# Kernel tuning notes

Hardware: AMD Instinct MI355X
Metric: run time of the kernel (lower is better)

## Reference

```python
import jax, jax.numpy as jnp
import numpy as np

B, N, D, F = 4, 4096, 1024, 64
LN_EPS = 1e-5
ATTN_EPS = 1e-6


def setup_inputs() -> dict:
    key = jax.random.key(0)
    ks = jax.random.split(key, 9)
    s = 0.02  # small init scale for weights
    return {
        "x": jax.random.normal(ks[0], (B, N, D), dtype=jnp.float32),
        "ln1_w": jnp.ones((D,), jnp.float32),
        "ln1_b": jnp.zeros((D,), jnp.float32),
        "q_w": jax.random.normal(ks[1], (F, D), jnp.float32) * s,
        "q_b": jnp.zeros((F,), jnp.float32),
        "k_w": jax.random.normal(ks[2], (F, D), jnp.float32) * s,
        "k_b": jnp.zeros((F,), jnp.float32),
        "v_w": jax.random.normal(ks[3], (D, D), jnp.float32) * s,
        "v_b": jnp.zeros((D,), jnp.float32),
        "o_w": jax.random.normal(ks[4], (D, D), jnp.float32) * s,
        "o_b": jnp.zeros((D,), jnp.float32),
        "ln2_w": jnp.ones((D,), jnp.float32),
        "ln2_b": jnp.zeros((D,), jnp.float32),
        "f1_w": jax.random.normal(ks[5], (4 * D, D), jnp.float32) * s,
        "f1_b": jnp.zeros((4 * D,), jnp.float32),
        "f2_w": jax.random.normal(ks[6], (D, 4 * D), jnp.float32) * s,
        "f2_b": jnp.zeros((D,), jnp.float32),
    }


def _layer_norm(x, w, b):
    mu = jnp.mean(x, axis=-1, keepdims=True)
    var = jnp.var(x, axis=-1, keepdims=True)
    return (x - mu) * jax.lax.rsqrt(var + LN_EPS) * w + b


def _linear(x, w, b):
    # torch nn.Linear convention: y = x @ w.T + b, w: [out, in]
    return jnp.einsum('bnd,fd->bnf', x, w) + b


def _causal_linear_attn(Q, K, V, eps=ATTN_EPS):
    """Q,K: [B,N,F] positive features; V: [B,N,D]. Recurrent causal scan."""
    b, n, f = K.shape
    d = V.shape[-1]
    Qt = jnp.swapaxes(Q, 0, 1)  # [N,B,F]
    Kt = jnp.swapaxes(K, 0, 1)
    Vt = jnp.swapaxes(V, 0, 1)  # [N,B,D]

    def step(carry, qkv):
        KV, Ks = carry  # [B,F,D], [B,F]
        q, k, v = qkv
        KV = KV + k[:, :, None] * v[:, None, :]
        Ks = Ks + k
        num = jnp.einsum('bf,bfd->bd', q, KV)
        den = jnp.sum(q * Ks, axis=-1, keepdims=True) + eps
        return (KV, Ks), num / den

    init = (jnp.zeros((b, f, d), Q.dtype), jnp.zeros((b, f), Q.dtype))
    _, out = jax.lax.scan(step, init, (Qt, Kt, Vt))
    return jnp.swapaxes(out, 0, 1)  # [B,N,D]


def reference(x, ln1_w, ln1_b, q_w, q_b, k_w, k_b, v_w, v_b,
              o_w, o_b, ln2_w, ln2_b, f1_w, f1_b, f2_w, f2_b):
    x_norm = _layer_norm(x, ln1_w, ln1_b)
    # LinearHopfieldASA, causal=True
    Q = jax.nn.elu(_linear(x_norm, q_w, q_b)) + 1.0  # positive feature map
    K = jax.nn.elu(_linear(x_norm, k_w, k_b)) + 1.0
    V = _linear(x_norm, v_w, v_b)
    attn = _causal_linear_attn(Q, K, V)
    attn = _linear(attn, o_w, o_b)
    x = x + attn
    h = _layer_norm(x, ln2_w, ln2_b)
    h = jax.nn.gelu(_linear(h, f1_w, f1_b), approximate=False)
    x = x + _linear(h, f2_w, f2_b)
    return x
```

## Files before the change

### kernel.cpp

```cpp
#include <hip/hip_runtime.h>
#include <hip/hip_bf16.h>
#include <cstdint>
#include <cstddef>


typedef __attribute__((ext_vector_type(8))) short short8;
typedef __attribute__((ext_vector_type(4))) short short4v;
typedef __attribute__((ext_vector_type(4))) float floatx4;
typedef __attribute__((ext_vector_type(4))) unsigned short ushort4v;

#define DEV static __device__ __forceinline__

DEV float b2f(unsigned short u) {
    union { unsigned int i; float f; } v; v.i = ((unsigned int)u) << 16; return v.f;
}
DEV unsigned short f2b(float f) {
    union { float f; unsigned int i; } v; v.f = f;
    unsigned int i = v.i;
    unsigned int r = (i + 0x7FFFu + ((i >> 16) & 1u)) >> 16;
    return (unsigned short)r;
}

DEV void gl_lds16(const void* g, void* l) {
    __builtin_amdgcn_global_load_lds((const __attribute__((address_space(1))) void*)g,
                                     (__attribute__((address_space(3))) void*)l, 16, 0, 0);
}

__global__ void eel_prep(const float* __restrict__ qw, const float* __restrict__ kw,
                         const float* __restrict__ vw, const float* __restrict__ ow,
                         const float* __restrict__ f1w, const float* __restrict__ f2w,
                         const float* __restrict__ qb, const float* __restrict__ kb,
                         const float* __restrict__ vb,
                         uint16_t* __restrict__ Wqkv, uint16_t* __restrict__ Wo,
                         uint16_t* __restrict__ W1, uint16_t* __restrict__ W2,
                         float* __restrict__ bqkv)
{
    size_t i = (size_t)blockIdx.x * 256 + threadIdx.x;
    size_t stride = (size_t)gridDim.x * 256;
    for (size_t t = i; t < 1152u * 1024u; t += stride) {
        int r = (int)(t >> 10);
        float v = (r < 64) ? qw[t] : (r < 128) ? kw[t - 65536] : vw[t - 131072];
        Wqkv[t] = f2b(v);
    }
    for (size_t t = i; t < 1048576u; t += stride) Wo[t] = f2b(ow[t]);
    for (size_t t = i; t < 4194304u; t += stride) { W1[t] = f2b(f1w[t]); W2[t] = f2b(f2w[t]); }
    if (i < 1152) bqkv[i] = (i < 64) ? qb[i] : (i < 128) ? kb[i - 64] : vb[i - 128];
}

__global__ __launch_bounds__(256) void eel_ln(const float* __restrict__ x,
                                              const float* __restrict__ w,
                                              const float* __restrict__ b,
                                              uint16_t* __restrict__ out)
{
    int row = blockIdx.x, tid = threadIdx.x;
    float4 xv = ((const float4*)(x + (size_t)row * 1024))[tid];
    float s  = xv.x + xv.y + xv.z + xv.w;
    float s2 = xv.x*xv.x + xv.y*xv.y + xv.z*xv.z + xv.w*xv.w;
#pragma unroll
    for (int off = 32; off > 0; off >>= 1) {
        s  += __shfl_down(s, off);
        s2 += __shfl_down(s2, off);
    }
    __shared__ float ps[8];
    int wv = tid >> 6;
    if ((tid & 63) == 0) { ps[wv] = s; ps[4 + wv] = s2; }
    __syncthreads();
    float mu  = (ps[0] + ps[1] + ps[2] + ps[3]) * (1.0f / 1024.0f);
    float var = (ps[4] + ps[5] + ps[6] + ps[7]) * (1.0f / 1024.0f) - mu * mu;
    float rs = rsqrtf(var + 1e-5f);
    float4 wv4 = ((const float4*)w)[tid];
    float4 bv4 = ((const float4*)b)[tid];
    ushort4v o;
    o.x = f2b((xv.x - mu) * rs * wv4.x + bv4.x);
    o.y = f2b((xv.y - mu) * rs * wv4.y + bv4.y);
    o.z = f2b((xv.z - mu) * rs * wv4.z + bv4.z);
    o.w = f2b((xv.w - mu) * rs * wv4.w + bv4.w);
    *(ushort4v*)(out + (size_t)row * 1024 + tid * 4) = o;
}

#define BM 128
#define BN 128
#define BKK 64

__global__ __launch_bounds__(256, 2) void eel_gemm(
    const uint16_t* __restrict__ A, int lda,
    const uint16_t* __restrict__ Bm, int ldb,
    int K,
    const float* __restrict__ bias,
    const float* __restrict__ res,
    uint16_t* __restrict__ outb,
    float* __restrict__ outf,
    int ldc, int mode)
{
    __shared__ uint16_t As[BM * BKK];
    __shared__ uint16_t Bs[BN * BKK];
    int tid = threadIdx.x;
    int lane = tid & 63, w = tid >> 6;
    int m0 = blockIdx.x * BM, n0 = blockIdx.y * BN;
    int wr = (w >> 1) * 64, wc = (w & 1) * 64;
    int quad = lane >> 4, l16 = lane & 15;
    floatx4 acc[4][4] = {};

    int nkb = K / BKK;
    for (int kb = 0; kb < nkb; ++kb) {
        int k0 = kb * BKK;
#pragma unroll
        for (int it = 0; it < 4; ++it) {
            int seg = it * 256 + tid;
            int row = seg >> 3, sub = seg & 7;
            int gs = sub ^ (row & 7);
            gl_lds16(A + (size_t)(m0 + row) * lda + k0 + gs * 8, (char*)As + seg * 16);
            gl_lds16(Bm + (size_t)(n0 + row) * ldb + k0 + gs * 8, (char*)Bs + seg * 16);
        }
        __syncthreads();
#pragma unroll
        for (int ks = 0; ks < 2; ++ks) {
            short8 a[4], b[4];
#pragma unroll
            for (int i = 0; i < 4; i++) {
                int mrow = wr + i * 16 + l16;
                int sa = (ks * 4 + quad) ^ (mrow & 7);
                a[i] = *(const short8*)((const char*)As + mrow * (BKK * 2) + sa * 16);
                int nrow = wc + i * 16 + l16;
                int sb = (ks * 4 + quad) ^ (nrow & 7);
                b[i] = *(const short8*)((const char*)Bs + nrow * (BKK * 2) + sb * 16);
            }
#pragma unroll
            for (int i = 0; i < 4; i++)
#pragma unroll
                for (int j = 0; j < 4; j++)
                    acc[i][j] = __builtin_amdgcn_mfma_f32_16x16x32_bf16(a[i], b[j], acc[i][j], 0, 0, 0);
        }
        __syncthreads();
    }

#pragma unroll
    for (int j = 0; j < 4; j++) {
        int col = n0 + wc + j * 16 + l16;
        float bv = bias[col];
#pragma unroll
        for (int i = 0; i < 4; i++) {
#pragma unroll
            for (int r = 0; r < 4; r++) {
                int row = m0 + wr + i * 16 + quad * 4 + r;
                float v = acc[i][j][r] + bv;
                size_t off = (size_t)row * ldc + col;
                if (mode == 0) {
                    if (col < 128) v = (v > 0.f) ? v + 1.f : __expf(v);
                    outb[off] = f2b(v);
                } else if (mode == 1) {
                    outf[off] = v + res[off];
                } else {
                    float u = 0.7978845608028654f * v * (1.0f + 0.044715f * v * v);
                    float e = __expf(2.0f * u);
                    float t = 1.0f - 2.0f / (e + 1.0f);
                    v = 0.5f * v * (1.0f + t);
                    outb[off] = f2b(v);
                }
            }
        }
    }
}

__global__ __launch_bounds__(256) void eel_attn_s(
    const uint16_t* __restrict__ QKV,
    uint16_t* __restrict__ Sg,
    float* __restrict__ den,
    float* __restrict__ KsA)
{
    int chunk = blockIdx.x, tid = threadIdx.x;
    int tok0 = chunk * 64;
    __shared__ uint16_t Q[64 * 64];
    __shared__ uint16_t Kc[64 * 64];
    __shared__ float denp[64][4];
    {
        int nloc = tid >> 2, seg = tid & 3;
        const uint16_t* src = QKV + (size_t)(tok0 + nloc) * 1152 + seg * 16;
        *(short8*)(Q + nloc * 64 + seg * 16)     = *(const short8*)(src);
        *(short8*)(Q + nloc * 64 + seg * 16 + 8) = *(const short8*)(src + 8);
        src += 64;
        *(short8*)(Kc + nloc * 64 + seg * 16)     = *(const short8*)(src);
        *(short8*)(Kc + nloc * 64 + seg * 16 + 8) = *(const short8*)(src + 8);
    }
    __syncthreads();
    if (tid < 64) {
        float s = 0.f;
        for (int m = 0; m < 64; m++) s += b2f(Kc[m * 64 + tid]);
        KsA[chunk * 64 + tid] = s;
    }
    int n = tid >> 2, mg = tid & 3;
    float dsum = 0.f;
    for (int mi = 0; mi < 16; mi++) {
        int m = mg * 16 + mi;
        size_t soff = (size_t)(tok0 + n) * 64 + m;
        if (m <= n) {
            float s = 0.f;
#pragma unroll
            for (int f = 0; f < 64; f += 8) {
                short8 q8 = *(const short8*)(Q + n * 64 + f);
                short8 k8 = *(const short8*)(Kc + m * 64 + f);
#pragma unroll
                for (int j = 0; j < 8; j++)
                    s += b2f((unsigned short)q8[j]) * b2f((unsigned short)k8[j]);
            }
            dsum += s;
            Sg[soff] = f2b(s);
        } else {
            Sg[soff] = 0;
        }
    }
    denp[n][mg] = dsum;
    __syncthreads();
    if (tid < 64)
        den[tok0 + tid] = denp[tid][0] + denp[tid][1] + denp[tid][2] + denp[tid][3];
}

__global__ __launch_bounds__(256) void eel_attn_kv(
    const uint16_t* __restrict__ QKV,
    float* __restrict__ KV_A)
{
    int bi = blockIdx.x;
    int chunk = bi >> 3, p = bi & 7;
    int tid = threadIdx.x;
    int tok0 = chunk * 64;
    __shared__ uint16_t Kc[64 * 64];
    __shared__ uint16_t Vp[64 * 128];
    {
        int r = tid >> 2, sg = tid & 3;
        const uint16_t* src = QKV + (size_t)(tok0 + r) * 1152 + 64 + sg * 16;
        *(short8*)(Kc + r * 64 + sg * 16)     = *(const short8*)(src);
        *(short8*)(Kc + r * 64 + sg * 16 + 8) = *(const short8*)(src + 8);
    }
#pragma unroll
    for (int it = 0; it < 2; it++) {
        int s = it * 256 + tid;
        int r = s >> 3, sub = s & 7;
        const uint16_t* src = QKV + (size_t)(tok0 + r) * 1152 + 128 + p * 128 + sub * 16;
        *(short8*)(Vp + r * 128 + sub * 16)     = *(const short8*)(src);
        *(short8*)(Vp + r * 128 + sub * 16 + 8) = *(const short8*)(src + 8);
    }
    __syncthreads();
    int f0 = (tid >> 5) * 8, d0 = (tid & 31) * 4;
    float acc[8][4] = {};
#pragma unroll 2
    for (int m = 0; m < 64; m++) {
        short8 k8 = *(const short8*)(Kc + m * 64 + f0);
        short4v v4 = *(const short4v*)(Vp + m * 128 + d0);
        float v0 = b2f((unsigned short)v4[0]), v1 = b2f((unsigned short)v4[1]);
        float v2 = b2f((unsigned short)v4[2]), v3 = b2f((unsigned short)v4[3]);
#pragma unroll
        for (int i = 0; i < 8; i++) {
            float kk = b2f((unsigned short)k8[i]);
            acc[i][0] += kk * v0; acc[i][1] += kk * v1;
            acc[i][2] += kk * v2; acc[i][3] += kk * v3;
        }
    }
#pragma unroll
    for (int i = 0; i < 8; i++) {
        float4 st = { acc[i][0], acc[i][1], acc[i][2], acc[i][3] };
        *(float4*)(KV_A + ((size_t)chunk * 64 + f0 + i) * 1024 + p * 128 + d0) = st;
    }
}

__global__ __launch_bounds__(256) void eel_kv_prefix(
    const float* __restrict__ KV_A, uint16_t* __restrict__ KV_P)
{
    int bi = blockIdx.x;
    int b = bi >> 8, rem = bi & 255;
    int f = rem >> 2;
    int d = (rem & 3) * 256 + threadIdx.x;
    float acc = 0.f;
    for (int cc = 0; cc < 64; cc++) {
        size_t idx = (((size_t)(b * 64 + cc)) * 64 + f) * 1024 + d;
        KV_P[idx] = f2b(acc);
        acc += KV_A[idx];
    }
}

__global__ void eel_ks_prefix(const float* __restrict__ KsA, float* __restrict__ KsP)
{
    int b = blockIdx.x, f = threadIdx.x;
    float acc = 0.f;
    for (int cc = 0; cc < 64; cc++) {
        int idx = (b * 64 + cc) * 64 + f;
        KsP[idx] = acc;
        acc += KsA[idx];
    }
}

__global__ __launch_bounds__(256) void eel_attn_out(
    const uint16_t* __restrict__ QKV,
    const uint16_t* __restrict__ Sg,
    const float* __restrict__ den,
    const float* __restrict__ KsP,
    const uint16_t* __restrict__ KV_P,
    uint16_t* __restrict__ attn)
{
    int bi = blockIdx.x;
    int chunk = bi >> 3, p = bi & 7;
    int tid = threadIdx.x;
    int tok0 = chunk * 64;
    __shared__ uint16_t Qt[64 * 64];
    __shared__ uint16_t St[64 * 64];
    __shared__ uint16_t Vp[64 * 128];
    __shared__ uint16_t KVp[64 * 128];
    __shared__ float dfull[64];
    {
        int n = tid >> 2, fs = (tid & 3) * 16;
        const uint16_t* qsrc = QKV + (size_t)(tok0 + n) * 1152 + fs;
        short8 a0 = *(const short8*)(qsrc);
        short8 a1 = *(const short8*)(qsrc + 8);
        const uint16_t* ssrc = Sg + (size_t)(tok0 + n) * 64 + fs;
        short8 s0 = *(const short8*)(ssrc);
        short8 s1 = *(const short8*)(ssrc + 8);
#pragma unroll
        for (int j = 0; j < 8; j++) {
            Qt[(fs + j) * 64 + n]     = (unsigned short)a0[j];
            Qt[(fs + 8 + j) * 64 + n] = (unsigned short)a1[j];
            St[(fs + j) * 64 + n]     = (unsigned short)s0[j];
            St[(fs + 8 + j) * 64 + n] = (unsigned short)s1[j];
        }
    }
#pragma unroll
    for (int it = 0; it < 2; it++) {
        int s = it * 256 + tid;
        int r = s >> 3, sub = s & 7;
        const uint16_t* vsrc = QKV + (size_t)(tok0 + r) * 1152 + 128 + p * 128 + sub * 16;
        *(short8*)(Vp + r * 128 + sub * 16)     = *(const short8*)(vsrc);
        *(short8*)(Vp + r * 128 + sub * 16 + 8) = *(const short8*)(vsrc + 8);
        const uint16_t* kvsrc = KV_P + ((size_t)(chunk * 64 + r)) * 1024 + p * 128 + sub * 16;
        *(short8*)(KVp + r * 128 + sub * 16)     = *(const short8*)(kvsrc);
        *(short8*)(KVp + r * 128 + sub * 16 + 8) = *(const short8*)(kvsrc + 8);
    }
    __syncthreads();
    if (tid < 64) {
        float s = 0.f;
        for (int f = 0; f < 64; f++)
            s += b2f(Qt[f * 64 + tid]) * KsP[chunk * 64 + f];
        dfull[tid] = s + den[tok0 + tid] + 1e-6f;
    }
    __syncthreads();
    int n0 = (tid >> 5) * 8, d0 = (tid & 31) * 4;
    float acc[8][4] = {};
#pragma unroll 2
    for (int f = 0; f < 64; f++) {
        short8 q8 = *(const short8*)(Qt + f * 64 + n0);
        short4v kv4 = *(const short4v*)(KVp + f * 128 + d0);
        float v0 = b2f((unsigned short)kv4[0]), v1 = b2f((unsigned short)kv4[1]);
        float v2 = b2f((unsigned short)kv4[2]), v3 = b2f((unsigned short)kv4[3]);
#pragma unroll
        for (int i = 0; i < 8; i++) {
            float q = b2f((unsigned short)q8[i]);
            acc[i][0] += q * v0; acc[i][1] += q * v1;
            acc[i][2] += q * v2; acc[i][3] += q * v3;
        }
    }
#pragma unroll 2
    for (int m = 0; m < 64; m++) {
        short8 s8 = *(const short8*)(St + m * 64 + n0);
        short4v v4 = *(const short4v*)(Vp + m * 128 + d0);
        float v0 = b2f((unsigned short)v4[0]), v1 = b2f((unsigned short)v4[1]);
        float v2 = b2f((unsigned short)v4[2]), v3 = b2f((unsigned short)v4[3]);
#pragma unroll
        for (int i = 0; i < 8; i++) {
            float q = b2f((unsigned short)s8[i]);
            acc[i][0] += q * v0; acc[i][1] += q * v1;
            acc[i][2] += q * v2; acc[i][3] += q * v3;
        }
    }
#pragma unroll
    for (int i = 0; i < 8; i++) {
        int n = n0 + i;
        float rinv = 1.0f / dfull[n];
        ushort4v st;
        st.x = f2b(acc[i][0] * rinv);
        st.y = f2b(acc[i][1] * rinv);
        st.z = f2b(acc[i][2] * rinv);
        st.w = f2b(acc[i][3] * rinv);
        *(ushort4v*)(attn + (size_t)(tok0 + n) * 1024 + p * 128 + d0) = st;
    }
}

extern "C" void kernel_launch(void* const* d_in, const int* in_sizes, int n_in,
                              void* d_out, int out_size, void* d_ws, size_t ws_size,
                              hipStream_t stream)
{
    (void)in_sizes; (void)n_in; (void)out_size; (void)ws_size;
    const float* x     = (const float*)d_in[0];
    const float* ln1w  = (const float*)d_in[1];
    const float* ln1b  = (const float*)d_in[2];
    const float* qw    = (const float*)d_in[3];
    const float* qb    = (const float*)d_in[4];
    const float* kw    = (const float*)d_in[5];
    const float* kb    = (const float*)d_in[6];
    const float* vw    = (const float*)d_in[7];
    const float* vb    = (const float*)d_in[8];
    const float* ow    = (const float*)d_in[9];
    const float* ob    = (const float*)d_in[10];
    const float* ln2w  = (const float*)d_in[11];
    const float* ln2b  = (const float*)d_in[12];
    const float* f1w   = (const float*)d_in[13];
    const float* f1b   = (const float*)d_in[14];
    const float* f2w   = (const float*)d_in[15];
    const float* f2bs  = (const float*)d_in[16];
    float* out = (float*)d_out;
    char* ws = (char*)d_ws;

    const size_t o_Wqkv = 0;
    const size_t o_Wo   = o_Wqkv + 2359296;
    const size_t o_W1   = o_Wo   + 2097152;
    const size_t o_W2   = o_W1   + 8388608;
    const size_t o_bqkv = o_W2   + 8388608;
    const size_t O_XN   = 21238272;
    const size_t O_QKV  = 54792704;
    const size_t O_S    = 92541440;
    const size_t O_DEN  = 94638592;
    const size_t O_KSA  = 94704128;
    const size_t O_KSP  = 94769664;
    const size_t O_KVA  = 94835200;
    const size_t O_KVP  = 161944064;

    uint16_t* Wqkv  = (uint16_t*)(ws + o_Wqkv);
    uint16_t* Wo    = (uint16_t*)(ws + o_Wo);
    uint16_t* W1    = (uint16_t*)(ws + o_W1);
    uint16_t* W2    = (uint16_t*)(ws + o_W2);
    float*    bqkv  = (float*)(ws + o_bqkv);
    uint16_t* xn    = (uint16_t*)(ws + O_XN);
    uint16_t* attn  = (uint16_t*)(ws + O_XN);
    uint16_t* QKV   = (uint16_t*)(ws + O_QKV);
    uint16_t* hnorm = (uint16_t*)(ws + O_QKV);
    uint16_t* Sg    = (uint16_t*)(ws + O_S);
    float*    den   = (float*)(ws + O_DEN);
    float*    KsA   = (float*)(ws + O_KSA);
    float*    KsP   = (float*)(ws + O_KSP);
    float*    KV_A  = (float*)(ws + O_KVA);
    uint16_t* hbuf  = (uint16_t*)(ws + O_KVA);
    uint16_t* KV_P  = (uint16_t*)(ws + O_KVP);

    eel_prep<<<4096, 256, 0, stream>>>(qw, kw, vw, ow, f1w, f2w, qb, kb, vb,
                                       Wqkv, Wo, W1, W2, bqkv);
    eel_ln<<<16384, 256, 0, stream>>>(x, ln1w, ln1b, xn);
    eel_gemm<<<dim3(128, 9), 256, 0, stream>>>(xn, 1024, Wqkv, 1024, 1024,
                                               bqkv, nullptr, QKV, nullptr, 1152, 0);
    eel_attn_s<<<256, 256, 0, stream>>>(QKV, Sg, den, KsA);
    eel_attn_kv<<<2048, 256, 0, stream>>>(QKV, KV_A);
    eel_kv_prefix<<<1024, 256, 0, stream>>>(KV_A, KV_P);
    eel_ks_prefix<<<4, 64, 0, stream>>>(KsA, KsP);
    eel_attn_out<<<2048, 256, 0, stream>>>(QKV, Sg, den, KsP, KV_P, attn);
    eel_gemm<<<dim3(128, 8), 256, 0, stream>>>(attn, 1024, Wo, 1024, 1024,
                                               ob, x, nullptr, out, 1024, 1);
    eel_ln<<<16384, 256, 0, stream>>>(out, ln2w, ln2b, hnorm);
    for (int half = 0; half < 2; half++) {
        size_t roff = (size_t)half * 8192;
        eel_gemm<<<dim3(64, 32), 256, 0, stream>>>(hnorm + roff * 1024, 1024, W1, 1024, 1024,
                                                   f1b, nullptr, hbuf, nullptr, 4096, 2);
        eel_gemm<<<dim3(64, 8), 256, 0, stream>>>(hbuf, 4096, W2, 4096, 4096,
                                                  f2bs, out + roff * 1024, nullptr,
                                                  out + roff * 1024, 1024, 1);
    }
}
```

Baseline: 867.6 us.

## Split FFN over hidden-dim strips and store per-chunk KV partials in bf16

```diff
diff --git a/kernel.cpp b/kernel.cpp
--- a/kernel.cpp
+++ b/kernel.cpp
@@ -137,7 +137,7 @@
 #pragma unroll
     for (int j = 0; j < 4; j++) {
         int col = n0 + wc + j * 16 + l16;
-        float bv = bias[col];
+        float bv = bias ? bias[col] : 0.0f;
 #pragma unroll
         for (int i = 0; i < 4; i++) {
 #pragma unroll
@@ -217,7 +217,7 @@
 
 __global__ __launch_bounds__(256) void eel_attn_kv(
     const uint16_t* __restrict__ QKV,
-    float* __restrict__ KV_A)
+    uint16_t* __restrict__ KV_A)
 {
     int bi = blockIdx.x;
     int chunk = bi >> 3, p = bi & 7;
@@ -257,13 +257,15 @@
     }
 #pragma unroll
     for (int i = 0; i < 8; i++) {
-        float4 st = { acc[i][0], acc[i][1], acc[i][2], acc[i][3] };
-        *(float4*)(KV_A + ((size_t)chunk * 64 + f0 + i) * 1024 + p * 128 + d0) = st;
+        ushort4v st;
+        st.x = f2b(acc[i][0]); st.y = f2b(acc[i][1]);
+        st.z = f2b(acc[i][2]); st.w = f2b(acc[i][3]);
+        *(ushort4v*)(KV_A + ((size_t)chunk * 64 + f0 + i) * 1024 + p * 128 + d0) = st;
     }
 }
 
 __global__ __launch_bounds__(256) void eel_kv_prefix(
-    const float* __restrict__ KV_A, uint16_t* __restrict__ KV_P)
+    const uint16_t* __restrict__ KV_A, uint16_t* __restrict__ KV_P)
 {
     int bi = blockIdx.x;
     int b = bi >> 8, rem = bi & 255;
@@ -273,7 +275,7 @@
     for (int cc = 0; cc < 64; cc++) {
         size_t idx = (((size_t)(b * 64 + cc)) * 64 + f) * 1024 + d;
         KV_P[idx] = f2b(acc);
-        acc += KV_A[idx];
+        acc += b2f(KV_A[idx]);
     }
 }
 
@@ -433,7 +435,7 @@
     float*    den   = (float*)(ws + O_DEN);
     float*    KsA   = (float*)(ws + O_KSA);
     float*    KsP   = (float*)(ws + O_KSP);
-    float*    KV_A  = (float*)(ws + O_KVA);
+    uint16_t* KV_A  = (uint16_t*)(ws + O_KVA);
     uint16_t* hbuf  = (uint16_t*)(ws + O_KVA);
     uint16_t* KV_P  = (uint16_t*)(ws + O_KVP);
 
@@ -450,12 +452,12 @@
     eel_gemm<<<dim3(128, 8), 256, 0, stream>>>(attn, 1024, Wo, 1024, 1024,
                                                ob, x, nullptr, out, 1024, 1);
     eel_ln<<<16384, 256, 0, stream>>>(out, ln2w, ln2b, hnorm);
-    for (int half = 0; half < 2; half++) {
-        size_t roff = (size_t)half * 8192;
-        eel_gemm<<<dim3(64, 32), 256, 0, stream>>>(hnorm + roff * 1024, 1024, W1, 1024, 1024,
-                                                   f1b, nullptr, hbuf, nullptr, 4096, 2);
-        eel_gemm<<<dim3(64, 8), 256, 0, stream>>>(hbuf, 4096, W2, 4096, 4096,
-                                                  f2bs, out + roff * 1024, nullptr,
-                                                  out + roff * 1024, 1024, 1);
-    }
-}
+    for (int strip = 0; strip < 2; strip++) {
+        size_t noff = (size_t)strip * 2048;
+        eel_gemm<<<dim3(128, 16), 256, 0, stream>>>(hnorm, 1024, W1 + noff * 1024, 1024, 1024,
+                                                    f1b + noff, nullptr, hbuf, nullptr, 2048, 2);
+        eel_gemm<<<dim3(128, 8), 256, 0, stream>>>(hbuf, 2048, W2 + noff, 4096, 2048,
+                                                   strip == 0 ? f2bs : nullptr, out, nullptr,
+                                                   out, 1024, 1);
+    }
+}
```

Result: slower. 904.6 us (+4.3%).
